# Kernel optimization log

Hardware: AMD Instinct MI355X
Metric: run time of the kernel (lower is better)

Reference implementation:

```python
import jax, jax.numpy as jnp
import numpy as np

N, E, EL = 20000, 320000, 100000
IN, HID, OUT, H = 256, 128, 128, 4
NEG_SLOPE = 0.2


def setup_inputs() -> dict:
    key = jax.random.key(0)
    ks = jax.random.split(key, 20)
    g = lambda k, shape, fan: jax.random.normal(k, shape, jnp.float32) * (1.0 / np.sqrt(fan))
    inp = {
        'x': jax.random.normal(ks[0], (N, IN), jnp.float32),
        'edge_index': jax.random.randint(ks[1], (2, E), 0, N, jnp.int32),
        'edge_label_index': jax.random.randint(ks[2], (2, EL), 0, N, jnp.int32),
        # GATv2 layer 1: in -> hidden, heads=H, concat
        'W_l1': g(ks[3], (IN, H * HID), IN), 'b_l1': jnp.zeros((H * HID,), jnp.float32),
        'W_r1': g(ks[4], (IN, H * HID), IN), 'b_r1': jnp.zeros((H * HID,), jnp.float32),
        'att1': g(ks[5], (H, HID), HID), 'bias1': jnp.zeros((H * HID,), jnp.float32),
        # GATv2 layer 2: H*hidden -> out, heads=1
        'W_l2': g(ks[6], (H * HID, OUT), H * HID), 'b_l2': jnp.zeros((OUT,), jnp.float32),
        'W_r2': g(ks[7], (H * HID, OUT), H * HID), 'b_r2': jnp.zeros((OUT,), jnp.float32),
        'att2': g(ks[8], (1, OUT), OUT), 'bias2': jnp.zeros((OUT,), jnp.float32),
        # decoder: Linear(2*OUT, HID) -> GELU -> Linear(HID, 1)
        'W_d1': g(ks[9], (2 * OUT, HID), 2 * OUT), 'b_d1': jnp.zeros((HID,), jnp.float32),
        'W_d2': g(ks[10], (HID, 1), HID), 'b_d2': jnp.zeros((1,), jnp.float32),
    }
    return inp


def gatv2_conv(x, src, dst, Wl, bl, Wr, br, att, bias, heads, ch):
    n = x.shape[0]
    xl = (x @ Wl + bl).reshape(n, heads, ch)  # source transform
    xr = (x @ Wr + br).reshape(n, heads, ch)  # target transform
    xj = xl[src]                              # [E, H, C] messages from source
    xi = xr[dst]                              # [E, H, C]
    e = jax.nn.leaky_relu(xi + xj, NEG_SLOPE)
    logits = jnp.einsum('ehc,hc->eh', e, att)  # [E, H]
    # segment softmax over incoming edges of each target node
    m = jax.ops.segment_max(logits, dst, num_segments=n)
    a = jnp.exp(logits - m[dst])
    s = jax.ops.segment_sum(a, dst, num_segments=n)
    alpha = a / s[dst]
    out = jax.ops.segment_sum(alpha[..., None] * xj, dst, num_segments=n)
    return out.reshape(n, heads * ch) + bias


def reference(x, edge_index, edge_label_index,
              W_l1, b_l1, W_r1, b_r1, att1, bias1,
              W_l2, b_l2, W_r2, b_r2, att2, bias2,
              W_d1, b_d1, W_d2, b_d2):
    n = x.shape[0]
    loops = jnp.arange(n, dtype=edge_index.dtype)
    src = jnp.concatenate([edge_index[0], loops])  # add_self_loops=True (PyG default)
    dst = jnp.concatenate([edge_index[1], loops])
    z = gatv2_conv(x, src, dst, W_l1, b_l1, W_r1, b_r1, att1, bias1, H, HID)
    z = jax.nn.gelu(z)  # dropout is identity in eval mode
    z = gatv2_conv(z, src, dst, W_l2, b_l2, W_r2, b_r2, att2, bias2, 1, OUT)
    # link decoder: gather-concat-MLP
    h = jnp.concatenate([z[edge_label_index[0]], z[edge_label_index[1]]], axis=-1)
    h = jax.nn.gelu(h @ W_d1 + b_d1)
    return (h @ W_d2 + b_d2).squeeze(-1)
```

## Files before the change

kernel.cpp:

```cpp
#include <hip/hip_runtime.h>
#include <hip/hip_bf16.h>
#include <math.h>
#include <stdint.h>

using bf16 = __hip_bfloat16;
typedef unsigned short u16;
typedef unsigned int   u32;
typedef __attribute__((ext_vector_type(8))) short short8;
typedef __attribute__((ext_vector_type(4))) float f32x4;
typedef _Float16 h2 __attribute__((ext_vector_type(2)));

static constexpr int NN   = 20000;
static constexpr int EE   = 320000;
static constexpr int ELN  = 100000;
static constexpr int ETOT = EE + NN;
static constexpr int INC  = 256;
static constexpr int C1   = 512;
static constexpr int C2   = 128;
static constexpr int NB   = (NN + 255) / 256;

__device__ __forceinline__ float us2f(u16 u){ union{u32 i; float f;}x; x.i=((u32)u)<<16; return x.f; }
__device__ __forceinline__ u16  f2us(float f){ union{bf16 h; u16 u;}c; c.h=__float2bfloat16(f); return c.u; }
__device__ __forceinline__ float h2f(u16 u){ union{u16 u; _Float16 h;}c; c.u=u; return (float)c.h; }
__device__ __forceinline__ float gelu_f(float x){
  float u = 1.5957691216057308f*(x + 0.044715f*x*x*x);
  float ex = __expf(u);
  float th = 1.f - 2.f/(ex + 1.f);
  return 0.5f*x*(1.f+th);
}
__device__ __forceinline__ void gl_lds16(const u16* g, void* l) {
  __builtin_amdgcn_global_load_lds((const __attribute__((address_space(1))) void*)g,
                                   (__attribute__((address_space(3))) void*)l, 16, 0, 0);
}
__device__ __forceinline__ void ld4v(const float* p, float* o){ float4 v=*(const float4*)p; o[0]=v.x;o[1]=v.y;o[2]=v.z;o[3]=v.w; }
__device__ __forceinline__ void ld4v(const u16* p, float* o){ uint2 v=*(const uint2*)p;
  o[0]=us2f(v.x&0xffff);o[1]=us2f(v.x>>16);o[2]=us2f(v.y&0xffff);o[3]=us2f(v.y>>16); }
__device__ __forceinline__ void ld4v(const _Float16* p, float* o){ uint2 v=*(const uint2*)p;
  o[0]=h2f(v.x&0xffff);o[1]=h2f(v.x>>16);o[2]=h2f(v.y&0xffff);o[3]=h2f(v.y>>16); }
__device__ __forceinline__ void ld8v(const float* p, float* o){ ld4v(p,o); ld4v(p+4,o+4); }
__device__ __forceinline__ void ld8v(const u16* p, float* o){ uint4 v=*(const uint4*)p;
  o[0]=us2f(v.x&0xffff);o[1]=us2f(v.x>>16);o[2]=us2f(v.y&0xffff);o[3]=us2f(v.y>>16);
  o[4]=us2f(v.z&0xffff);o[5]=us2f(v.z>>16);o[6]=us2f(v.w&0xffff);o[7]=us2f(v.w>>16); }
__device__ __forceinline__ void ld8v(const _Float16* p, float* o){ uint4 v=*(const uint4*)p;
  o[0]=h2f(v.x&0xffff);o[1]=h2f(v.x>>16);o[2]=h2f(v.y&0xffff);o[3]=h2f(v.y>>16);
  o[4]=h2f(v.z&0xffff);o[5]=h2f(v.z>>16);o[6]=h2f(v.w&0xffff);o[7]=h2f(v.w>>16); }
__device__ __forceinline__ void ld2v(const float* p, float* o){ float2 v=*(const float2*)p; o[0]=v.x;o[1]=v.y; }
__device__ __forceinline__ void ld2v(const _Float16* p, float* o){ u32 w=*(const u32*)p;
  o[0]=h2f(w&0xffff); o[1]=h2f(w>>16); }
__device__ __forceinline__ void st4v(float* p, const float* v){ *(float4*)p = make_float4(v[0],v[1],v[2],v[3]); }
__device__ __forceinline__ void st4v(u16* p, const float* v){ uint2 o;
  o.x=f2us(v[0])|((u32)f2us(v[1])<<16); o.y=f2us(v[2])|((u32)f2us(v[3])<<16); *(uint2*)p=o; }
__device__ __forceinline__ void st8v(float* p, const float* v){ st4v(p,v); st4v(p+4,v+4); }
__device__ __forceinline__ void st8v(u16* p, const float* v){ uint4 o;
  o.x=f2us(v[0])|((u32)f2us(v[1])<<16); o.y=f2us(v[2])|((u32)f2us(v[3])<<16);
  o.z=f2us(v[4])|((u32)f2us(v[5])<<16); o.w=f2us(v[6])|((u32)f2us(v[7])<<16); *(uint4*)p=o; }

__global__ void k_hist(const int* __restrict__ ei, int* __restrict__ cnt) {
  int e = blockIdx.x*blockDim.x + threadIdx.x;
  if (e < ETOT) {
    int d = (e < EE) ? ei[EE + e] : (e - EE);
    if ((u32)d < (u32)NN) atomicAdd(&cnt[d], 1);
  }
}
__global__ void k_scan_a(const int* __restrict__ cnt, int* __restrict__ row_ptr,
                         int* __restrict__ bsum) {
  __shared__ int buf[256];
  int idx = blockIdx.x*256 + threadIdx.x;
  int v = (idx < NN) ? cnt[idx] : 0;
  buf[threadIdx.x] = v;
  __syncthreads();
  for (int off = 1; off < 256; off <<= 1) {
    int t = (threadIdx.x >= off) ? buf[threadIdx.x - off] : 0;
    __syncthreads();
    buf[threadIdx.x] += t;
    __syncthreads();
  }
  if (idx < NN) row_ptr[idx] = buf[threadIdx.x] - v;
  if (threadIdx.x == 255) bsum[blockIdx.x] = buf[255];
}
__global__ void k_scan_b(int* __restrict__ bsum, int* __restrict__ row_ptr) {
  __shared__ int buf[128];
  int v = (threadIdx.x < NB) ? bsum[threadIdx.x] : 0;
  buf[threadIdx.x] = v;
  __syncthreads();
  for (int off = 1; off < 128; off <<= 1) {
    int t = (threadIdx.x >= off) ? buf[threadIdx.x - off] : 0;
    __syncthreads();
    buf[threadIdx.x] += t;
    __syncthreads();
  }
  if (threadIdx.x < NB) bsum[threadIdx.x] = buf[threadIdx.x] - v;
  if (threadIdx.x == 127) row_ptr[NN] = buf[127];
}
__global__ void k_scan_c(int* __restrict__ row_ptr, const int* __restrict__ bsum,
                         int* __restrict__ cur) {
  int idx = blockIdx.x*256 + threadIdx.x;
  if (idx < NN) {
    int v = row_ptr[idx] + bsum[blockIdx.x];
    row_ptr[idx] = v;
    cur[idx] = v;
  }
}
__global__ void k_scatter(const int* __restrict__ ei, int* __restrict__ cur,
                          int* __restrict__ col) {
  int e = blockIdx.x*blockDim.x + threadIdx.x;
  if (e < ETOT) {
    int s, d;
    if (e < EE) { s = ei[e]; d = ei[EE + e]; } else { s = d = e - EE; }
    if ((u32)d >= (u32)NN) d = 0;
    int pos = atomicAdd(&cur[d], 1);
    if ((u32)pos < (u32)ETOT) col[pos] = s;
  }
}

__global__ __launch_bounds__(256) void k_xsplit(const float* __restrict__ A,
                                                u16* __restrict__ Ath, u16* __restrict__ Atl,
                                                int n) {
  for (int i = blockIdx.x*256 + threadIdx.x; i < n; i += gridDim.x*256) {
    float v = A[i];
    u16 h = f2us(v);
    Ath[i] = h;
    Atl[i] = f2us(v - us2f(h));
  }
}

struct WsArgs { const float* src[5]; u16* th[5]; u16* tl[5]; int K[5]; int N[5]; };
__global__ __launch_bounds__(256) void k_wsplit_all(WsArgs a) {
  int seg = blockIdx.y;
  int K = a.K[seg], N = a.N[seg];
  int n = K * N;
  int idx = blockIdx.x*256 + threadIdx.x;
  if (idx >= n) return;
  int nn = idx / K, k = idx - nn*K;
  float v = a.src[seg][(size_t)k*N + nn];
  u16 h = f2us(v);
  a.th[seg][idx] = h;
  a.tl[seg][idx] = f2us(v - us2f(h));
}

__global__ __launch_bounds__(256, 3)
void k_mgemm_a(const u16* __restrict__ Ath, const u16* __restrict__ Atl,
               const u16* __restrict__ Bth, const u16* __restrict__ Btl,
               const float* __restrict__ biasA, const float* __restrict__ biasB, int ncut,
               _Float16* __restrict__ C, int M, int N, int K, int nby) {
  __shared__ __align__(16) u16 sm[17408];
  int tid = threadIdx.x;
  int bidy = blockIdx.x % nby, bidx = blockIdx.x / nby;
  int m0 = bidx * 128, n0 = bidy * 128;
  int wave = tid >> 6, lane = tid & 63;
  int wm = (wave & 1) * 64, wn = (wave >> 1) * 64;
  int l15 = lane & 15, quad = lane >> 4;
  const u16* pbase = (wave == 0) ? Ath : (wave == 1) ? Atl : (wave == 2) ? Bth : Btl;
  bool isA = wave < 2;
  int rbase = isA ? m0 : n0;
  int rseg = lane >> 2;
  int kseg = (lane & 3) * 8;
  f32x4 acc[4][4] = {};
  for (int k0 = 0; k0 < K; k0 += 32) {
    #pragma unroll
    for (int i = 0; i < 8; ++i) {
      int r = rbase + i*16 + rseg;
      if (isA && r > M-1) r = M-1;
      gl_lds16(&pbase[(size_t)r*K + k0 + kseg], (char*)sm + (wave<<13) + (i<<10));
    }
    __syncthreads();
    short8 af_h[4], af_l[4], bf_h[4], bf_l[4];
    #pragma unroll
    for (int i = 0; i < 4; ++i) {
      af_h[i] = *(const short8*)&sm[         (wm + i*16 + l15)*32 + quad*8];
      af_l[i] = *(const short8*)&sm[ 4096 +  (wm + i*16 + l15)*32 + quad*8];
      bf_h[i] = *(const short8*)&sm[ 8192 +  (wn + i*16 + l15)*32 + quad*8];
      bf_l[i] = *(const short8*)&sm[12288 +  (wn + i*16 + l15)*32 + quad*8];
    }
    #pragma unroll
    for (int i = 0; i < 4; ++i)
      #pragma unroll
      for (int j = 0; j < 4; ++j) {
        acc[i][j] = __builtin_amdgcn_mfma_f32_16x16x32_bf16(af_h[i], bf_l[j], acc[i][j], 0,0,0);
        acc[i][j] = __builtin_amdgcn_mfma_f32_16x16x32_bf16(af_l[i], bf_h[j], acc[i][j], 0,0,0);
        acc[i][j] = __builtin_amdgcn_mfma_f32_16x16x32_bf16(af_h[i], bf_h[j], acc[i][j], 0,0,0);
      }
    __syncthreads();
  }
  #pragma unroll
  for (int j = 0; j < 4; ++j) {
    int col = wn + j*16 + l15;
    int colg = n0 + col;
    float bv = (colg < ncut) ? biasA[colg] : biasB[colg - ncut];
    #pragma unroll
    for (int i = 0; i < 4; ++i) {
      int rowb = wm + i*16 + quad*4;
      #pragma unroll
      for (int r = 0; r < 4; ++r) {
        union { _Float16 h; u16 u; } cv;
        cv.h = (_Float16)(acc[i][j][r] + bv);
        sm[(rowb + r)*136 + col] = cv.u;
      }
    }
  }
  __syncthreads();
  int row = tid >> 1, half = (tid & 1) * 64;
  int gr = m0 + row;
  if (gr < M) {
    uint4* d = (uint4*)&C[(size_t)gr*N + n0 + half];
    const uint4* s = (const uint4*)&sm[row*136 + half];
    #pragma unroll
    for (int q = 0; q < 8; ++q) d[q] = s[q];
  }
}

__global__ __launch_bounds__(256, 2)
void k_dec3(const _Float16* __restrict__ z2,
            const int* __restrict__ eli,
            const u16* __restrict__ Wth, const u16* __restrict__ Wtl,
            const float* __restrict__ bd1,
            const float* __restrict__ Wd2, const float* __restrict__ bd2,
            float* __restrict__ out) {
  __shared__ __align__(16) u16 Ah[128][32], Al[128][32];
  __shared__ __align__(16) u16 Bh[128][32], Bl[128][32];
  __shared__ float pr[128][2];
  int tid = threadIdx.x;
  int e0 = blockIdx.x * 128;
  int wave = tid >> 6, lane = tid & 63;
  int wm = (wave & 1) * 64, wn = (wave >> 1) * 64;
  int l15 = lane & 15, quad = lane >> 4;
  int ar = tid >> 3;
  int ak = (tid & 7) * 4;
  int bn = tid >> 2;
  int bc = (tid & 3) * 8;
  int ia4[4], ib4[4];
  #pragma unroll
  for (int i = 0; i < 4; ++i) {
    int e = e0 + ar + 32*i;
    bool ev = e < ELN;
    int a = ev ? eli[e] : 0;      if ((u32)a >= (u32)NN) a = 0;
    int b = ev ? eli[ELN+e] : 0;  if ((u32)b >= (u32)NN) b = 0;
    ia4[i] = a; ib4[i] = b;
  }
  f32x4 acc[4][4] = {};
  for (int k0 = 0; k0 < 256; k0 += 32) {
    #pragma unroll
    for (int i = 0; i < 4; ++i) {
      int row = ar + 32*i;
      int kk = k0 + ak;
      const _Float16* src = (kk < 128) ? &z2[(size_t)ia4[i]*128 + kk]
                                       : &z2[(size_t)ib4[i]*128 + (kk - 128)];
      float hv[4];
      ld4v(src, hv);
      u16 hi[4], lo[4];
      #pragma unroll
      for (int j = 0; j < 4; ++j) {
        hi[j] = f2us(hv[j]);
        lo[j] = f2us(hv[j] - us2f(hi[j]));
      }
      *(uint2*)&Ah[row][ak] = make_uint2(hi[0]|((u32)hi[1]<<16), hi[2]|((u32)hi[3]<<16));
      *(uint2*)&Al[row][ak] = make_uint2(lo[0]|((u32)lo[1]<<16), lo[2]|((u32)lo[3]<<16));
    }
    #pragma unroll
    for (int i = 0; i < 2; ++i) {
      int n = bn + 64*i;
      *(uint4*)&Bh[n][bc] = *(const uint4*)&Wth[(size_t)n*256 + k0 + bc];
      *(uint4*)&Bl[n][bc] = *(const uint4*)&Wtl[(size_t)n*256 + k0 + bc];
    }
    __syncthreads();
    short8 af_h[4], af_l[4], bf_h[4], bf_l[4];
    #pragma unroll
    for (int i = 0; i < 4; ++i) {
      af_h[i] = *(const short8*)&Ah[wm + i*16 + l15][quad*8];
      af_l[i] = *(const short8*)&Al[wm + i*16 + l15][quad*8];
      bf_h[i] = *(const short8*)&Bh[wn + i*16 + l15][quad*8];
      bf_l[i] = *(const short8*)&Bl[wn + i*16 + l15][quad*8];
    }
    #pragma unroll
    for (int i = 0; i < 4; ++i)
      #pragma unroll
      for (int j = 0; j < 4; ++j) {
        acc[i][j] = __builtin_amdgcn_mfma_f32_16x16x32_bf16(af_h[i], bf_l[j], acc[i][j], 0,0,0);
        acc[i][j] = __builtin_amdgcn_mfma_f32_16x16x32_bf16(af_l[i], bf_h[j], acc[i][j], 0,0,0);
        acc[i][j] = __builtin_amdgcn_mfma_f32_16x16x32_bf16(af_h[i], bf_h[j], acc[i][j], 0,0,0);
      }
    __syncthreads();
  }
  float w2c[4], bbc[4];
  #pragma unroll
  for (int j = 0; j < 4; ++j) {
    int col = wn + j*16 + l15;
    w2c[j] = Wd2[col];
    bbc[j] = bd1[col];
  }
  #pragma unroll
  for (int i = 0; i < 4; ++i) {
    #pragma unroll
    for (int r = 0; r < 4; ++r) {
      float part = 0.f;
      #pragma unroll
      for (int j = 0; j < 4; ++j)
        part += gelu_f(acc[i][j][r] + bbc[j]) * w2c[j];
      part += __shfl_xor(part,1); part += __shfl_xor(part,2);
      part += __shfl_xor(part,4); part += __shfl_xor(part,8);
      if (l15 == 0) pr[wm + i*16 + quad*4 + r][wn>>6] = part;
    }
  }
  __syncthreads();
  if (tid < 128) {
    int e = e0 + tid;
    if (e < ELN) out[e] = pr[tid][0] + pr[tid][1] + bd2[0];
  }
}

__global__ __launch_bounds__(256) void k_edge1p(const _Float16* __restrict__ xl,
                                                const _Float16* __restrict__ xr, int ld,
                                                const float* __restrict__ att,
                                                const float* __restrict__ bias,
                                                const int* __restrict__ row_ptr,
                                                const int* __restrict__ col,
                                                u16* __restrict__ z1h, u16* __restrict__ z1l) {
  int wid = (blockIdx.x*blockDim.x + threadIdx.x) >> 6;
  if (wid >= NN) return;
  int lane = threadIdx.x & 63;
  int c8 = lane*8;
  union Q { uint4 u; h2 h[4]; };
  Q XI; XI.u = *(const uint4*)&xr[(size_t)wid*ld + c8];
  h2 at[4];
  #pragma unroll
  for (int k=0;k<4;++k) { at[k][0] = (_Float16)att[c8+2*k]; at[k][1] = (_Float16)att[c8+2*k+1]; }
  const h2 k02 = {(_Float16)0.2f, (_Float16)0.2f};
  float acc[8] = {};
  float s = 0.f;
  int e0 = __builtin_amdgcn_readfirstlane(row_ptr[wid]);
  int e1 = __builtin_amdgcn_readfirstlane(row_ptr[wid+1]);
  int e = e0;
  if ((e1 - e0) & 1) {
    int sn = __builtin_amdgcn_readfirstlane(col[e]); if ((u32)sn >= (u32)NN) sn = 0;
    Q XJ; XJ.u = *(const uint4*)&xl[(size_t)sn*ld + c8];
    float p = 0.f;
    #pragma unroll
    for (int k=0;k<4;++k) {
      h2 t = XI.h[k] + XJ.h[k];
      t = __builtin_elementwise_max(t, t*k02);
      p = __builtin_amdgcn_fdot2(t, at[k], p, false);
    }
    p += __shfl_xor(p,1); p += __shfl_xor(p,2);
    p += __shfl_xor(p,4); p += __shfl_xor(p,8);
    float w = __expf(p);
    s += w;
    #pragma unroll
    for (int k=0;k<4;++k) {
      acc[2*k]   += w*(float)XJ.h[k][0];
      acc[2*k+1] += w*(float)XJ.h[k][1];
    }
    ++e;
  }
  for (; e < e1; e += 2) {
    int s1 = __builtin_amdgcn_readfirstlane(col[e]);   if ((u32)s1 >= (u32)NN) s1 = 0;
    int s2 = __builtin_amdgcn_readfirstlane(col[e+1]); if ((u32)s2 >= (u32)NN) s2 = 0;
    Q X1, X2;
    X1.u = *(const uint4*)&xl[(size_t)s1*ld + c8];
    X2.u = *(const uint4*)&xl[(size_t)s2*ld + c8];
    float p1 = 0.f, p2 = 0.f;
    #pragma unroll
    for (int k=0;k<4;++k) {
      h2 t1 = XI.h[k] + X1.h[k];
      t1 = __builtin_elementwise_max(t1, t1*k02);
      p1 = __builtin_amdgcn_fdot2(t1, at[k], p1, false);
      h2 t2 = XI.h[k] + X2.h[k];
      t2 = __builtin_elementwise_max(t2, t2*k02);
      p2 = __builtin_amdgcn_fdot2(t2, at[k], p2, false);
    }
    p1 += __shfl_xor(p1,1); p2 += __shfl_xor(p2,1);
    p1 += __shfl_xor(p1,2); p2 += __shfl_xor(p2,2);
    p1 += __shfl_xor(p1,4); p2 += __shfl_xor(p2,4);
    p1 += __shfl_xor(p1,8); p2 += __shfl_xor(p2,8);
    float w1 = __expf(p1);
    float w2 = __expf(p2);
    s += w1 + w2;
    #pragma unroll
    for (int k=0;k<4;++k) {
      acc[2*k]   += w1*(float)X1.h[k][0] + w2*(float)X2.h[k][0];
      acc[2*k+1] += w1*(float)X1.h[k][1] + w2*(float)X2.h[k][1];
    }
  }
  float inv = 1.f/s;
  u16 hh[8], ll[8];
  #pragma unroll
  for (int j=0;j<8;++j) {
    float o = gelu_f(acc[j]*inv + bias[c8+j]);
    hh[j] = f2us(o);
    ll[j] = f2us(o - us2f(hh[j]));
  }
  uint4 H, L;
  H.x = hh[0]|((u32)hh[1]<<16); H.y = hh[2]|((u32)hh[3]<<16);
  H.z = hh[4]|((u32)hh[5]<<16); H.w = hh[6]|((u32)hh[7]<<16);
  L.x = ll[0]|((u32)ll[1]<<16); L.y = ll[2]|((u32)ll[3]<<16);
  L.z = ll[4]|((u32)ll[5]<<16); L.w = ll[6]|((u32)ll[7]<<16);
  *(uint4*)&z1h[(size_t)wid*C1 + c8] = H;
  *(uint4*)&z1l[(size_t)wid*C1 + c8] = L;
}

__global__ __launch_bounds__(256) void k_edge2p(const _Float16* __restrict__ xl,
                                                const _Float16* __restrict__ xr, int ld,
                                                const float* __restrict__ att,
                                                const float* __restrict__ bias,
                                                const int* __restrict__ row_ptr,
                                                const int* __restrict__ col,
                                                _Float16* __restrict__ z2) {
  int wid = (blockIdx.x*blockDim.x + threadIdx.x) >> 6;
  if (wid >= NN) return;
  int lane = threadIdx.x & 63;
  int c2 = lane*2;
  union W { u32 u; h2 h; };
  W XI; XI.u = *(const u32*)&xr[(size_t)wid*ld + c2];
  h2 at; at[0] = (_Float16)att[c2]; at[1] = (_Float16)att[c2+1];
  const h2 k02 = {(_Float16)0.2f, (_Float16)0.2f};
  float s = 0.f, ac0 = 0.f, ac1 = 0.f;
  int e0 = __builtin_amdgcn_readfirstlane(row_ptr[wid]);
  int e1 = __builtin_amdgcn_readfirstlane(row_ptr[wid+1]);
  int e = e0;
  if ((e1 - e0) & 1) {
    int sn = __builtin_amdgcn_readfirstlane(col[e]); if ((u32)sn >= (u32)NN) sn = 0;
    W XJ; XJ.u = *(const u32*)&xl[(size_t)sn*ld + c2];
    h2 t = XI.h + XJ.h;
    t = __builtin_elementwise_max(t, t*k02);
    float p = __builtin_amdgcn_fdot2(t, at, 0.f, false);
    p += __shfl_xor(p,1);  p += __shfl_xor(p,2);
    p += __shfl_xor(p,4);  p += __shfl_xor(p,8);
    p += __shfl_xor(p,16); p += __shfl_xor(p,32);
    float w = __expf(p);
    s += w;
    ac0 += w*(float)XJ.h[0];
    ac1 += w*(float)XJ.h[1];
    ++e;
  }
  for (; e < e1; e += 2) {
    int s1 = __builtin_amdgcn_readfirstlane(col[e]);   if ((u32)s1 >= (u32)NN) s1 = 0;
    int s2 = __builtin_amdgcn_readfirstlane(col[e+1]); if ((u32)s2 >= (u32)NN) s2 = 0;
    W X1, X2;
    X1.u = *(const u32*)&xl[(size_t)s1*ld + c2];
    X2.u = *(const u32*)&xl[(size_t)s2*ld + c2];
    h2 t1 = XI.h + X1.h;
    t1 = __builtin_elementwise_max(t1, t1*k02);
    float p1 = __builtin_amdgcn_fdot2(t1, at, 0.f, false);
    h2 t2 = XI.h + X2.h;
    t2 = __builtin_elementwise_max(t2, t2*k02);
    float p2 = __builtin_amdgcn_fdot2(t2, at, 0.f, false);
    p1 += __shfl_xor(p1,1);  p2 += __shfl_xor(p2,1);
    p1 += __shfl_xor(p1,2);  p2 += __shfl_xor(p2,2);
    p1 += __shfl_xor(p1,4);  p2 += __shfl_xor(p2,4);
    p1 += __shfl_xor(p1,8);  p2 += __shfl_xor(p2,8);
    p1 += __shfl_xor(p1,16); p2 += __shfl_xor(p2,16);
    p1 += __shfl_xor(p1,32); p2 += __shfl_xor(p2,32);
    float w1 = __expf(p1);
    float w2 = __expf(p2);
    s += w1 + w2;
    ac0 += w1*(float)X1.h[0] + w2*(float)X2.h[0];
    ac1 += w1*(float)X1.h[1] + w2*(float)X2.h[1];
  }
  float inv = 1.f/s;
  union { h2 h; u32 u; } o;
  o.h[0] = (_Float16)(ac0*inv + bias[c2]);
  o.h[1] = (_Float16)(ac1*inv + bias[c2+1]);
  *(u32*)&z2[(size_t)wid*C2 + c2] = o.u;
}

template <typename AT, typename CT>
__global__ __launch_bounds__(256) void k_gemm(const AT* __restrict__ A,
                                              const float* __restrict__ W,
                                              const float* __restrict__ bias,
                                              CT* __restrict__ C,
                                              int M, int Nc, int K) {
  __shared__ __align__(16) float As[16][64];
  __shared__ __align__(16) float Bs[16][64];
  int tid = threadIdx.x;
  int m0 = blockIdx.x*64, n0 = blockIdx.y*64;
  int ty = tid >> 4, tx = tid & 15;
  int lrow = tid >> 2;
  int lk   = (tid & 3)*4;
  int wk   = tid >> 4;
  int wn   = (tid & 15)*4;
  float acc[4][4] = {};
  for (int k0 = 0; k0 < K; k0 += 16) {
    int row = m0 + lrow;
    if (row < M) {
      float a4[4]; ld4v(&A[(size_t)row*K + k0 + lk], a4);
      As[lk+0][lrow]=a4[0]; As[lk+1][lrow]=a4[1]; As[lk+2][lrow]=a4[2]; As[lk+3][lrow]=a4[3];
    } else {
      #pragma unroll
      for (int j=0;j<4;++j) As[lk+j][lrow]=0.f;
    }
    {
      float4 bv4 = *(const float4*)&W[(size_t)(k0+wk)*Nc + n0 + wn];
      Bs[wk][wn+0]=bv4.x; Bs[wk][wn+1]=bv4.y; Bs[wk][wn+2]=bv4.z; Bs[wk][wn+3]=bv4.w;
    }
    __syncthreads();
    #pragma unroll
    for (int kk=0;kk<16;++kk) {
      float4 av = *(const float4*)&As[kk][ty*4];
      float4 bv = *(const float4*)&Bs[kk][tx*4];
      float a[4]={av.x,av.y,av.z,av.w}, b[4]={bv.x,bv.y,bv.z,bv.w};
      #pragma unroll
      for (int i=0;i<4;++i)
        #pragma unroll
        for (int j=0;j<4;++j)
          acc[i][j] += a[i]*b[j];
    }
    __syncthreads();
  }
  float bv[4];
  #pragma unroll
  for (int j=0;j<4;++j) bv[j] = bias[n0 + tx*4 + j];
  #pragma unroll
  for (int i=0;i<4;++i) {
    int row = m0 + ty*4 + i;
    if (row < M) {
      float o4[4] = {acc[i][0]+bv[0], acc[i][1]+bv[1], acc[i][2]+bv[2], acc[i][3]+bv[3]};
      st4v(&C[(size_t)row*Nc + n0 + tx*4], o4);
    }
  }
}

template <typename TI, typename TO>
__global__ __launch_bounds__(256) void k_edge1c(const TI* __restrict__ xl,
                                                const TI* __restrict__ xr, int ld,
                                                const float* __restrict__ att,
                                                const float* __restrict__ bias,
                                                const int* __restrict__ row_ptr,
                                                const int* __restrict__ col,
                                                TO* __restrict__ z1) {
  int wid = (blockIdx.x*blockDim.x + threadIdx.x) >> 6;
  if (wid >= NN) return;
  int lane = threadIdx.x & 63;
  int c8 = lane*8;
  float xi[8], av[8], acc[8] = {};
  ld8v(&xr[(size_t)wid*ld + c8], xi);
  #pragma unroll
  for (int j=0;j<8;++j) av[j] = att[c8+j];
  float s = 0.f;
  int e0 = row_ptr[wid], e1 = row_ptr[wid+1];
  for (int e = e0; e < e1; ++e) {
    int sn = col[e]; if ((u32)sn >= (u32)NN) sn = 0;
    float xj[8];
    ld8v(&xl[(size_t)sn*ld + c8], xj);
    float p = 0.f;
    #pragma unroll
    for (int j=0;j<8;++j) {
      float t = xi[j] + xj[j];
      t = fmaxf(t, 0.2f*t);
      p += t*av[j];
    }
    p += __shfl_xor(p,1); p += __shfl_xor(p,2);
    p += __shfl_xor(p,4); p += __shfl_xor(p,8);
    float w = __expf(p);
    s += w;
    #pragma unroll
    for (int j=0;j<8;++j) acc[j] += w*xj[j];
  }
  float inv = 1.f/s, o[8];
  #pragma unroll
  for (int j=0;j<8;++j) o[j] = gelu_f(acc[j]*inv + bias[c8+j]);
  st8v(&z1[(size_t)wid*C1 + c8], o);
}

template <typename TI, typename TO>
__global__ __launch_bounds__(256) void k_edge2c(const TI* __restrict__ xl,
                                                const TI* __restrict__ xr, int ld,
                                                const float* __restrict__ att,
                                                const float* __restrict__ bias,
                                                const int* __restrict__ row_ptr,
                                                const int* __restrict__ col,
                                                TO* __restrict__ z2) {
  int wid = (blockIdx.x*blockDim.x + threadIdx.x) >> 6;
  if (wid >= NN) return;
  int lane = threadIdx.x & 63;
  int c2 = lane*2;
  float xiv[2];
  ld2v(&xr[(size_t)wid*ld + c2], xiv);
  float a0 = att[c2], a1 = att[c2+1];
  float s = 0.f, ac0 = 0.f, ac1 = 0.f;
  int e0 = row_ptr[wid], e1 = row_ptr[wid+1];
  for (int e = e0; e < e1; ++e) {
    int sn = col[e]; if ((u32)sn >= (u32)NN) sn = 0;
    float xj[2];
    ld2v(&xl[(size_t)sn*ld + c2], xj);
    float t0 = xiv[0] + xj[0]; t0 = fmaxf(t0, 0.2f*t0);
    float t1 = xiv[1] + xj[1]; t1 = fmaxf(t1, 0.2f*t1);
    float p = t0*a0 + t1*a1;
    p += __shfl_xor(p,1);  p += __shfl_xor(p,2);
    p += __shfl_xor(p,4);  p += __shfl_xor(p,8);
    p += __shfl_xor(p,16); p += __shfl_xor(p,32);
    float w = __expf(p);
    s += w;
    ac0 += w*xj[0];
    ac1 += w*xj[1];
  }
  float inv = 1.f/s;
  z2[(size_t)wid*C2 + c2]   = (TO)(ac0*inv + bias[c2]);
  z2[(size_t)wid*C2 + c2+1] = (TO)(ac1*inv + bias[c2+1]);
}

__global__ __launch_bounds__(256) void k_dec2(const float* __restrict__ z2,
                                              const int* __restrict__ eli,
                                              const float* __restrict__ Wd1,
                                              const float* __restrict__ bd1,
                                              const float* __restrict__ Wd2,
                                              const float* __restrict__ bd2,
                                              float* __restrict__ out) {
  __shared__ __align__(16) float As[16][64];
  __shared__ __align__(16) float Bs[16][128];
  int tid = threadIdx.x;
  int e0 = blockIdx.x * 64;
  int ty = tid >> 4, tx = tid & 15;
  int lrow = tid >> 2;
  int lk   = (tid & 3) * 4;
  int wk   = tid >> 4;
  int wn   = (tid & 15) * 8;
  int e = e0 + lrow;
  bool ev = e < ELN;
  int ia = ev ? eli[e] : 0;       if ((u32)ia >= (u32)NN) ia = 0;
  int ib = ev ? eli[ELN+e] : 0;   if ((u32)ib >= (u32)NN) ib = 0;
  float acc[4][8] = {};
  for (int k0 = 0; k0 < 256; k0 += 16) {
    int kk4 = k0 + lk;
    const float* src = (kk4 < 128) ? &z2[(size_t)ia*128 + kk4]
                                   : &z2[(size_t)ib*128 + (kk4 - 128)];
    float4 a4 = ev ? *(const float4*)src : make_float4(0.f,0.f,0.f,0.f);
    As[lk+0][lrow]=a4.x; As[lk+1][lrow]=a4.y; As[lk+2][lrow]=a4.z; As[lk+3][lrow]=a4.w;
    *(float4*)&Bs[wk][wn]   = *(const float4*)&Wd1[(size_t)(k0+wk)*128 + wn];
    *(float4*)&Bs[wk][wn+4] = *(const float4*)&Wd1[(size_t)(k0+wk)*128 + wn + 4];
    __syncthreads();
    #pragma unroll
    for (int kk = 0; kk < 16; ++kk) {
      float4 av = *(const float4*)&As[kk][ty*4];
      float a[4] = {av.x, av.y, av.z, av.w};
      float4 b0 = *(const float4*)&Bs[kk][tx*4];
      float4 b1 = *(const float4*)&Bs[kk][64 + tx*4];
      float b[8] = {b0.x,b0.y,b0.z,b0.w,b1.x,b1.y,b1.z,b1.w};
      #pragma unroll
      for (int i = 0; i < 4; ++i)
        #pragma unroll
        for (int j = 0; j < 8; ++j)
          acc[i][j] += a[i]*b[j];
    }
    __syncthreads();
  }
  float w2[8], bb[8];
  #pragma unroll
  for (int j = 0; j < 4; ++j) {
    w2[j]   = Wd2[tx*4+j];      bb[j]   = bd1[tx*4+j];
    w2[j+4] = Wd2[64+tx*4+j];   bb[j+4] = bd1[64+tx*4+j];
  }
  float b2 = bd2[0];
  #pragma unroll
  for (int i = 0; i < 4; ++i) {
    float part = 0.f;
    #pragma unroll
    for (int j = 0; j < 8; ++j)
      part += gelu_f(acc[i][j] + bb[j]) * w2[j];
    part += __shfl_xor(part,1); part += __shfl_xor(part,2);
    part += __shfl_xor(part,4); part += __shfl_xor(part,8);
    int row = e0 + ty*4 + i;
    if (tx == 0 && row < ELN) out[row] = part + b2;
  }
}

__global__ void k_tiny(float* out, float code) {
  if (threadIdx.x == 0) out[0] = code;
}

extern "C" void kernel_launch(void* const* d_in, const int* in_sizes, int n_in,
                              void* d_out, int out_size, void* d_ws, size_t ws_size,
                              hipStream_t stream) {
  const float* x     = (const float*)d_in[0];
  const int*   ei    = (const int*)  d_in[1];
  const int*   eli   = (const int*)  d_in[2];
  const float* Wl1   = (const float*)d_in[3];
  const float* bl1   = (const float*)d_in[4];
  const float* Wr1   = (const float*)d_in[5];
  const float* br1   = (const float*)d_in[6];
  const float* att1  = (const float*)d_in[7];
  const float* bias1 = (const float*)d_in[8];
  const float* Wl2   = (const float*)d_in[9];
  const float* bl2   = (const float*)d_in[10];
  const float* Wr2   = (const float*)d_in[11];
  const float* br2   = (const float*)d_in[12];
  const float* att2  = (const float*)d_in[13];
  const float* bias2 = (const float*)d_in[14];
  const float* Wd1   = (const float*)d_in[15];
  const float* bd1   = (const float*)d_in[16];
  const float* Wd2   = (const float*)d_in[17];
  const float* bd2   = (const float*)d_in[18];
  float* out = (float*)d_out;

  constexpr size_t INTW = (size_t)(NN+1) + NN + ETOT;
  constexpr size_t FULL_WORDS = 3ull*NN*C1 + INTW;
  constexpr size_t CMP_WORDS  = 3ull*NN*C1/2 + INTW;

  bool full    = ws_size >= FULL_WORDS*4;
  bool compact = !full && ws_size >= CMP_WORDS*4;
  if (!full && !compact) {
    size_t mb = ws_size >> 20;
    k_tiny<<<1, 64, 0, stream>>>(out, 16384.f + (float)mb);
    return;
  }

  size_t regA = full ? (size_t)NN*C1 : (size_t)NN*C1/2;
  char* base = (char*)d_ws;
  void* wA = base;
  void* wB = base + regA*4;
  void* wC = base + 2*regA*4;
  int* row_ptr = (int*)(base + 3*regA*4);
  int* cnt     = row_ptr + (NN + 1);
  int* col     = cnt + NN;
  int* bsum    = (int*)wA;

  hipMemsetAsync(cnt, 0, NN*sizeof(int), stream);
  k_hist<<<(ETOT+255)/256, 256, 0, stream>>>(ei, cnt);
  k_scan_a<<<NB, 256, 0, stream>>>(cnt, row_ptr, bsum);
  k_scan_b<<<1, 128, 0, stream>>>(bsum, row_ptr);
  k_scan_c<<<NB, 256, 0, stream>>>(row_ptr, bsum, cnt);
  k_scatter<<<(ETOT+255)/256, 256, 0, stream>>>(ei, cnt, col);

  if (full) {
    _Float16* xlr1 = (_Float16*)wA;
    _Float16* xlr2 = (_Float16*)wA;
    u16* xth = (u16*)wB;
    u16* xtl = xth + (size_t)NN*INC;
    u16* wt1th = (u16*)((char*)wB + (21u<<20));
    u16* wt1tl = wt1th + 1024*256;
    u16* wt2th = wt1tl + 1024*256;
    u16* wt2tl = wt2th + 256*512;
    u16* wdth  = wt2tl + 256*512;
    u16* wdtl  = wdth  + 128*256;
    u16* z1h = (u16*)wC;
    u16* z1l = z1h + (size_t)NN*C1;
    _Float16* z2 = (_Float16*)wC;

    k_xsplit<<<2048, 256, 0, stream>>>(x, xth, xtl, NN*INC);
    WsArgs wa;
    wa.src[0]=Wl1; wa.th[0]=wt1th;          wa.tl[0]=wt1tl;          wa.K[0]=INC; wa.N[0]=C1;
    wa.src[1]=Wr1; wa.th[1]=wt1th+512*256;  wa.tl[1]=wt1tl+512*256;  wa.K[1]=INC; wa.N[1]=C1;
    wa.src[2]=Wl2; wa.th[2]=wt2th;          wa.tl[2]=wt2tl;          wa.K[2]=C1;  wa.N[2]=C2;
    wa.src[3]=Wr2; wa.th[3]=wt2th+128*512;  wa.tl[3]=wt2tl+128*512;  wa.K[3]=C1;  wa.N[3]=C2;
    wa.src[4]=Wd1; wa.th[4]=wdth;           wa.tl[4]=wdtl;           wa.K[4]=256; wa.N[4]=C2;
    k_wsplit_all<<<dim3(512, 5), 256, 0, stream>>>(wa);

    k_mgemm_a<<<157*8, 256, 0, stream>>>(xth, xtl, wt1th, wt1tl,
                                         bl1, br1, 512, xlr1, NN, 1024, INC, 8);
    k_edge1p<<<NN/4, 256, 0, stream>>>(xlr1, xlr1+512, 1024, att1, bias1, row_ptr, col, z1h, z1l);
    k_mgemm_a<<<157*2, 256, 0, stream>>>(z1h, z1l, wt2th, wt2tl,
                                         bl2, br2, 128, xlr2, NN, 256, C1, 2);
    k_edge2p<<<NN/4, 256, 0, stream>>>(xlr2, xlr2+128, 256, att2, bias2, row_ptr, col, z2);
    k_dec3<<<(ELN+127)/128, 256, 0, stream>>>(z2, eli, wdth, wdtl, bd1, Wd2, bd2, out);
  } else {
    u16* xl1 = (u16*)wA;
    u16* xr1 = (u16*)wB;
    u16* z1  = (u16*)wC;
    float* xl2 = (float*)wA;
    float* xr2 = (float*)wB;
    float* z2  = (float*)wC;
    dim3 g1((NN+63)/64, C1/64);
    dim3 g2((NN+63)/64, C2/64);
    k_gemm<float,u16><<<g1, 256, 0, stream>>>(x, Wl1, bl1, xl1, NN, C1, INC);
    k_gemm<float,u16><<<g1, 256, 0, stream>>>(x, Wr1, br1, xr1, NN, C1, INC);
    k_edge1c<u16,u16><<<NN/4, 256, 0, stream>>>(xl1, xr1, C1, att1, bias1, row_ptr, col, z1);
    k_gemm<u16,float><<<g2, 256, 0, stream>>>(z1, Wl2, bl2, xl2, NN, C2, C1);
    k_gemm<u16,float><<<g2, 256, 0, stream>>>(z1, Wr2, br2, xr2, NN, C2, C1);
    k_edge2c<float,float><<<NN/4, 256, 0, stream>>>(xl2, xr2, C2, att2, bias2, row_ptr, col, z2);
    k_dec2<<<(ELN+63)/64, 256, 0, stream>>>(z2, eli, Wd1, bd1, Wd2, bd2, out);
  }
}
```

Baseline: 359.2 us.

## Fuse prep kernels with histogram, unroll edge loops by four, raise dec3 occupancy

Folds the input split, the weight split and the edge-destination histogram into one grid-strided kernel, replacing three launches with one. The per-node edge loops in both GATv2 aggregation kernels move from a 2-way to a 4-way unroll with a scalar tail, keeping more gathers in flight. The decoder's launch-bounds occupancy hint goes from 2 to 3 blocks per SM, which may raise register pressure or cause spills. The fallback path keeps the separate histogram kernel.

```diff
diff --git a/kernel.cpp b/kernel.cpp
--- a/kernel.cpp
+++ b/kernel.cpp
@@ -55,13 +55,41 @@
   o.x=f2us(v[0])|((u32)f2us(v[1])<<16); o.y=f2us(v[2])|((u32)f2us(v[3])<<16);
   o.z=f2us(v[4])|((u32)f2us(v[5])<<16); o.w=f2us(v[6])|((u32)f2us(v[7])<<16); *(uint4*)p=o; }
 
-__global__ void k_hist(const int* __restrict__ ei, int* __restrict__ cnt) {
-  int e = blockIdx.x*blockDim.x + threadIdx.x;
-  if (e < ETOT) {
-    int d = (e < EE) ? ei[EE + e] : (e - EE);
-    if ((u32)d < (u32)NN) atomicAdd(&cnt[d], 1);
-  }
-}
+struct PrepArgs {
+  const float* x; u16* xth; u16* xtl; int nx;
+  const float* wsrc[5]; u16* wth[5]; u16* wtl[5]; int wK[5]; int wN[5];
+  const int* ei; int* cnt;
+};
+__global__ __launch_bounds__(256) void k_prep(PrepArgs a) {
+  int seg = blockIdx.y;
+  int tid = blockIdx.x*256 + threadIdx.x;
+  int stride = gridDim.x*256;
+  if (seg == 0) {
+    for (int i = tid; i < a.nx; i += stride) {
+      float v = a.x[i];
+      u16 h = f2us(v);
+      a.xth[i] = h;
+      a.xtl[i] = f2us(v - us2f(h));
+    }
+  } else if (seg <= 5) {
+    int s = seg - 1;
+    int K = a.wK[s], N = a.wN[s];
+    int n = K * N;
+    for (int i = tid; i < n; i += stride) {
+      int nn = i / K, k = i - nn*K;
+      float v = a.wsrc[s][(size_t)k*N + nn];
+      u16 h = f2us(v);
+      a.wth[s][i] = h;
+      a.wtl[s][i] = f2us(v - us2f(h));
+    }
+  } else {
+    for (int e = tid; e < ETOT; e += stride) {
+      int d = (e < EE) ? a.ei[EE + e] : (e - EE);
+      if ((u32)d < (u32)NN) atomicAdd(&a.cnt[d], 1);
+    }
+  }
+}
+
 __global__ void k_scan_a(const int* __restrict__ cnt, int* __restrict__ row_ptr,
                          int* __restrict__ bsum) {
   __shared__ int buf[256];
@@ -111,31 +139,6 @@
     int pos = atomicAdd(&cur[d], 1);
     if ((u32)pos < (u32)ETOT) col[pos] = s;
   }
-}
-
-__global__ __launch_bounds__(256) void k_xsplit(const float* __restrict__ A,
-                                                u16* __restrict__ Ath, u16* __restrict__ Atl,
-                                                int n) {
-  for (int i = blockIdx.x*256 + threadIdx.x; i < n; i += gridDim.x*256) {
-    float v = A[i];
-    u16 h = f2us(v);
-    Ath[i] = h;
-    Atl[i] = f2us(v - us2f(h));
-  }
-}
-
-struct WsArgs { const float* src[5]; u16* th[5]; u16* tl[5]; int K[5]; int N[5]; };
-__global__ __launch_bounds__(256) void k_wsplit_all(WsArgs a) {
-  int seg = blockIdx.y;
-  int K = a.K[seg], N = a.N[seg];
-  int n = K * N;
-  int idx = blockIdx.x*256 + threadIdx.x;
-  if (idx >= n) return;
-  int nn = idx / K, k = idx - nn*K;
-  float v = a.src[seg][(size_t)k*N + nn];
-  u16 h = f2us(v);
-  a.th[seg][idx] = h;
-  a.tl[seg][idx] = f2us(v - us2f(h));
 }
 
 __global__ __launch_bounds__(256, 3)
@@ -209,7 +212,7 @@
   }
 }
 
-__global__ __launch_bounds__(256, 2)
+__global__ __launch_bounds__(256, 3)
 void k_dec3(const _Float16* __restrict__ z2,
             const int* __restrict__ eli,
             const u16* __restrict__ Wth, const u16* __restrict__ Wtl,
@@ -330,7 +333,43 @@
   int e0 = __builtin_amdgcn_readfirstlane(row_ptr[wid]);
   int e1 = __builtin_amdgcn_readfirstlane(row_ptr[wid+1]);
   int e = e0;
-  if ((e1 - e0) & 1) {
+  for (; e + 4 <= e1; e += 4) {
+    int s1 = __builtin_amdgcn_readfirstlane(col[e]);   if ((u32)s1 >= (u32)NN) s1 = 0;
+    int s2 = __builtin_amdgcn_readfirstlane(col[e+1]); if ((u32)s2 >= (u32)NN) s2 = 0;
+    int s3 = __builtin_amdgcn_readfirstlane(col[e+2]); if ((u32)s3 >= (u32)NN) s3 = 0;
+    int s4 = __builtin_amdgcn_readfirstlane(col[e+3]); if ((u32)s4 >= (u32)NN) s4 = 0;
+    Q X1, X2, X3, X4;
+    X1.u = *(const uint4*)&xl[(size_t)s1*ld + c8];
+    X2.u = *(const uint4*)&xl[(size_t)s2*ld + c8];
+    X3.u = *(const uint4*)&xl[(size_t)s3*ld + c8];
+    X4.u = *(const uint4*)&xl[(size_t)s4*ld + c8];
+    float p1 = 0.f, p2 = 0.f, p3 = 0.f, p4 = 0.f;
+    #pragma unroll
+    for (int k=0;k<4;++k) {
+      h2 t1 = XI.h[k] + X1.h[k]; t1 = __builtin_elementwise_max(t1, t1*k02);
+      p1 = __builtin_amdgcn_fdot2(t1, at[k], p1, false);
+      h2 t2 = XI.h[k] + X2.h[k]; t2 = __builtin_elementwise_max(t2, t2*k02);
+      p2 = __builtin_amdgcn_fdot2(t2, at[k], p2, false);
+      h2 t3 = XI.h[k] + X3.h[k]; t3 = __builtin_elementwise_max(t3, t3*k02);
+      p3 = __builtin_amdgcn_fdot2(t3, at[k], p3, false);
+      h2 t4 = XI.h[k] + X4.h[k]; t4 = __builtin_elementwise_max(t4, t4*k02);
+      p4 = __builtin_amdgcn_fdot2(t4, at[k], p4, false);
+    }
+    p1 += __shfl_xor(p1,1); p2 += __shfl_xor(p2,1); p3 += __shfl_xor(p3,1); p4 += __shfl_xor(p4,1);
+    p1 += __shfl_xor(p1,2); p2 += __shfl_xor(p2,2); p3 += __shfl_xor(p3,2); p4 += __shfl_xor(p4,2);
+    p1 += __shfl_xor(p1,4); p2 += __shfl_xor(p2,4); p3 += __shfl_xor(p3,4); p4 += __shfl_xor(p4,4);
+    p1 += __shfl_xor(p1,8); p2 += __shfl_xor(p2,8); p3 += __shfl_xor(p3,8); p4 += __shfl_xor(p4,8);
+    float w1 = __expf(p1), w2 = __expf(p2), w3 = __expf(p3), w4 = __expf(p4);
+    s += (w1 + w2) + (w3 + w4);
+    #pragma unroll
+    for (int k=0;k<4;++k) {
+      acc[2*k]   += (w1*(float)X1.h[k][0] + w2*(float)X2.h[k][0])
+                  + (w3*(float)X3.h[k][0] + w4*(float)X4.h[k][0]);
+      acc[2*k+1] += (w1*(float)X1.h[k][1] + w2*(float)X2.h[k][1])
+                  + (w3*(float)X3.h[k][1] + w4*(float)X4.h[k][1]);
+    }
+  }
+  for (; e < e1; ++e) {
     int sn = __builtin_amdgcn_readfirstlane(col[e]); if ((u32)sn >= (u32)NN) sn = 0;
     Q XJ; XJ.u = *(const uint4*)&xl[(size_t)sn*ld + c8];
     float p = 0.f;
@@ -348,36 +387,6 @@
     for (int k=0;k<4;++k) {
       acc[2*k]   += w*(float)XJ.h[k][0];
       acc[2*k+1] += w*(float)XJ.h[k][1];
-    }
-    ++e;
-  }
-  for (; e < e1; e += 2) {
-    int s1 = __builtin_amdgcn_readfirstlane(col[e]);   if ((u32)s1 >= (u32)NN) s1 = 0;
-    int s2 = __builtin_amdgcn_readfirstlane(col[e+1]); if ((u32)s2 >= (u32)NN) s2 = 0;
-    Q X1, X2;
-    X1.u = *(const uint4*)&xl[(size_t)s1*ld + c8];
-    X2.u = *(const uint4*)&xl[(size_t)s2*ld + c8];
-    float p1 = 0.f, p2 = 0.f;
-    #pragma unroll
-    for (int k=0;k<4;++k) {
-      h2 t1 = XI.h[k] + X1.h[k];
-      t1 = __builtin_elementwise_max(t1, t1*k02);
-      p1 = __builtin_amdgcn_fdot2(t1, at[k], p1, false);
-      h2 t2 = XI.h[k] + X2.h[k];
-      t2 = __builtin_elementwise_max(t2, t2*k02);
-      p2 = __builtin_amdgcn_fdot2(t2, at[k], p2, false);
-    }
-    p1 += __shfl_xor(p1,1); p2 += __shfl_xor(p2,1);
-    p1 += __shfl_xor(p1,2); p2 += __shfl_xor(p2,2);
-    p1 += __shfl_xor(p1,4); p2 += __shfl_xor(p2,4);
-    p1 += __shfl_xor(p1,8); p2 += __shfl_xor(p2,8);
-    float w1 = __expf(p1);
-    float w2 = __expf(p2);
-    s += w1 + w2;
-    #pragma unroll
-    for (int k=0;k<4;++k) {
-      acc[2*k]   += w1*(float)X1.h[k][0] + w2*(float)X2.h[k][0];
-      acc[2*k+1] += w1*(float)X1.h[k][1] + w2*(float)X2.h[k][1];
     }
   }
   float inv = 1.f/s;
@@ -416,7 +425,36 @@
   int e0 = __builtin_amdgcn_readfirstlane(row_ptr[wid]);
   int e1 = __builtin_amdgcn_readfirstlane(row_ptr[wid+1]);
   int e = e0;
-  if ((e1 - e0) & 1) {
+  for (; e + 4 <= e1; e += 4) {
+    int s1 = __builtin_amdgcn_readfirstlane(col[e]);   if ((u32)s1 >= (u32)NN) s1 = 0;
+    int s2 = __builtin_amdgcn_readfirstlane(col[e+1]); if ((u32)s2 >= (u32)NN) s2 = 0;
+    int s3 = __builtin_amdgcn_readfirstlane(col[e+2]); if ((u32)s3 >= (u32)NN) s3 = 0;
+    int s4 = __builtin_amdgcn_readfirstlane(col[e+3]); if ((u32)s4 >= (u32)NN) s4 = 0;
+    W X1, X2, X3, X4;
+    X1.u = *(const u32*)&xl[(size_t)s1*ld + c2];
+    X2.u = *(const u32*)&xl[(size_t)s2*ld + c2];
+    X3.u = *(const u32*)&xl[(size_t)s3*ld + c2];
+    X4.u = *(const u32*)&xl[(size_t)s4*ld + c2];
+    h2 t1 = XI.h + X1.h; t1 = __builtin_elementwise_max(t1, t1*k02);
+    h2 t2 = XI.h + X2.h; t2 = __builtin_elementwise_max(t2, t2*k02);
+    h2 t3 = XI.h + X3.h; t3 = __builtin_elementwise_max(t3, t3*k02);
+    h2 t4 = XI.h + X4.h; t4 = __builtin_elementwise_max(t4, t4*k02);
+    float p1 = __builtin_amdgcn_fdot2(t1, at, 0.f, false);
+    float p2 = __builtin_amdgcn_fdot2(t2, at, 0.f, false);
+    float p3 = __builtin_amdgcn_fdot2(t3, at, 0.f, false);
+    float p4 = __builtin_amdgcn_fdot2(t4, at, 0.f, false);
+    p1 += __shfl_xor(p1,1);  p2 += __shfl_xor(p2,1);  p3 += __shfl_xor(p3,1);  p4 += __shfl_xor(p4,1);
+    p1 += __shfl_xor(p1,2);  p2 += __shfl_xor(p2,2);  p3 += __shfl_xor(p3,2);  p4 += __shfl_xor(p4,2);
+    p1 += __shfl_xor(p1,4);  p2 += __shfl_xor(p2,4);  p3 += __shfl_xor(p3,4);  p4 += __shfl_xor(p4,4);
+    p1 += __shfl_xor(p1,8);  p2 += __shfl_xor(p2,8);  p3 += __shfl_xor(p3,8);  p4 += __shfl_xor(p4,8);
+    p1 += __shfl_xor(p1,16); p2 += __shfl_xor(p2,16); p3 += __shfl_xor(p3,16); p4 += __shfl_xor(p4,16);
+    p1 += __shfl_xor(p1,32); p2 += __shfl_xor(p2,32); p3 += __shfl_xor(p3,32); p4 += __shfl_xor(p4,32);
+    float w1 = __expf(p1), w2 = __expf(p2), w3 = __expf(p3), w4 = __expf(p4);
+    s += (w1 + w2) + (w3 + w4);
+    ac0 += (w1*(float)X1.h[0] + w2*(float)X2.h[0]) + (w3*(float)X3.h[0] + w4*(float)X4.h[0]);
+    ac1 += (w1*(float)X1.h[1] + w2*(float)X2.h[1]) + (w3*(float)X3.h[1] + w4*(float)X4.h[1]);
+  }
+  for (; e < e1; ++e) {
     int sn = __builtin_amdgcn_readfirstlane(col[e]); if ((u32)sn >= (u32)NN) sn = 0;
     W XJ; XJ.u = *(const u32*)&xl[(size_t)sn*ld + c2];
     h2 t = XI.h + XJ.h;
@@ -429,31 +467,6 @@
     s += w;
     ac0 += w*(float)XJ.h[0];
     ac1 += w*(float)XJ.h[1];
-    ++e;
-  }
-  for (; e < e1; e += 2) {
-    int s1 = __builtin_amdgcn_readfirstlane(col[e]);   if ((u32)s1 >= (u32)NN) s1 = 0;
-    int s2 = __builtin_amdgcn_readfirstlane(col[e+1]); if ((u32)s2 >= (u32)NN) s2 = 0;
-    W X1, X2;
-    X1.u = *(const u32*)&xl[(size_t)s1*ld + c2];
-    X2.u = *(const u32*)&xl[(size_t)s2*ld + c2];
-    h2 t1 = XI.h + X1.h;
-    t1 = __builtin_elementwise_max(t1, t1*k02);
-    float p1 = __builtin_amdgcn_fdot2(t1, at, 0.f, false);
-    h2 t2 = XI.h + X2.h;
-    t2 = __builtin_elementwise_max(t2, t2*k02);
-    float p2 = __builtin_amdgcn_fdot2(t2, at, 0.f, false);
-    p1 += __shfl_xor(p1,1);  p2 += __shfl_xor(p2,1);
-    p1 += __shfl_xor(p1,2);  p2 += __shfl_xor(p2,2);
-    p1 += __shfl_xor(p1,4);  p2 += __shfl_xor(p2,4);
-    p1 += __shfl_xor(p1,8);  p2 += __shfl_xor(p2,8);
-    p1 += __shfl_xor(p1,16); p2 += __shfl_xor(p2,16);
-    p1 += __shfl_xor(p1,32); p2 += __shfl_xor(p2,32);
-    float w1 = __expf(p1);
-    float w2 = __expf(p2);
-    s += w1 + w2;
-    ac0 += w1*(float)X1.h[0] + w2*(float)X2.h[0];
-    ac1 += w1*(float)X1.h[1] + w2*(float)X2.h[1];
   }
   float inv = 1.f/s;
   union { h2 h; u32 u; } o;
@@ -462,6 +475,13 @@
   *(u32*)&z2[(size_t)wid*C2 + c2] = o.u;
 }
 
+__global__ void k_hist(const int* __restrict__ ei, int* __restrict__ cnt) {
+  int e = blockIdx.x*blockDim.x + threadIdx.x;
+  if (e < ETOT) {
+    int d = (e < EE) ? ei[EE + e] : (e - EE);
+    if ((u32)d < (u32)NN) atomicAdd(&cnt[d], 1);
+  }
+}
 template <typename AT, typename CT>
 __global__ __launch_bounds__(256) void k_gemm(const AT* __restrict__ A,
                                               const float* __restrict__ W,
@@ -517,7 +537,6 @@
     }
   }
 }
-
 template <typename TI, typename TO>
 __global__ __launch_bounds__(256) void k_edge1c(const TI* __restrict__ xl,
                                                 const TI* __restrict__ xr, int ld,
@@ -559,7 +578,6 @@
   for (int j=0;j<8;++j) o[j] = gelu_f(acc[j]*inv + bias[c8+j]);
   st8v(&z1[(size_t)wid*C1 + c8], o);
 }
-
 template <typename TI, typename TO>
 __global__ __launch_bounds__(256) void k_edge2c(const TI* __restrict__ xl,
                                                 const TI* __restrict__ xr, int ld,
@@ -596,7 +614,6 @@
   z2[(size_t)wid*C2 + c2]   = (TO)(ac0*inv + bias[c2]);
   z2[(size_t)wid*C2 + c2+1] = (TO)(ac1*inv + bias[c2+1]);
 }
-
 __global__ __launch_bounds__(256) void k_dec2(const float* __restrict__ z2,
                                               const int* __restrict__ eli,
                                               const float* __restrict__ Wd1,
@@ -713,11 +730,6 @@
   int* bsum    = (int*)wA;
 
   hipMemsetAsync(cnt, 0, NN*sizeof(int), stream);
-  k_hist<<<(ETOT+255)/256, 256, 0, stream>>>(ei, cnt);
-  k_scan_a<<<NB, 256, 0, stream>>>(cnt, row_ptr, bsum);
-  k_scan_b<<<1, 128, 0, stream>>>(bsum, row_ptr);
-  k_scan_c<<<NB, 256, 0, stream>>>(row_ptr, bsum, cnt);
-  k_scatter<<<(ETOT+255)/256, 256, 0, stream>>>(ei, cnt, col);
 
   if (full) {
     _Float16* xlr1 = (_Float16*)wA;
@@ -734,14 +746,20 @@
     u16* z1l = z1h + (size_t)NN*C1;
     _Float16* z2 = (_Float16*)wC;
 
-    k_xsplit<<<2048, 256, 0, stream>>>(x, xth, xtl, NN*INC);
-    WsArgs wa;
-    wa.src[0]=Wl1; wa.th[0]=wt1th;          wa.tl[0]=wt1tl;          wa.K[0]=INC; wa.N[0]=C1;
-    wa.src[1]=Wr1; wa.th[1]=wt1th+512*256;  wa.tl[1]=wt1tl+512*256;  wa.K[1]=INC; wa.N[1]=C1;
-    wa.src[2]=Wl2; wa.th[2]=wt2th;          wa.tl[2]=wt2tl;          wa.K[2]=C1;  wa.N[2]=C2;
-    wa.src[3]=Wr2; wa.th[3]=wt2th+128*512;  wa.tl[3]=wt2tl+128*512;  wa.K[3]=C1;  wa.N[3]=C2;
-    wa.src[4]=Wd1; wa.th[4]=wdth;           wa.tl[4]=wdtl;           wa.K[4]=256; wa.N[4]=C2;
-    k_wsplit_all<<<dim3(512, 5), 256, 0, stream>>>(wa);
+    PrepArgs pa;
+    pa.x = x; pa.xth = xth; pa.xtl = xtl; pa.nx = NN*INC;
+    pa.wsrc[0]=Wl1; pa.wth[0]=wt1th;         pa.wtl[0]=wt1tl;         pa.wK[0]=INC; pa.wN[0]=C1;
+    pa.wsrc[1]=Wr1; pa.wth[1]=wt1th+512*256; pa.wtl[1]=wt1tl+512*256; pa.wK[1]=INC; pa.wN[1]=C1;
+    pa.wsrc[2]=Wl2; pa.wth[2]=wt2th;         pa.wtl[2]=wt2tl;         pa.wK[2]=C1;  pa.wN[2]=C2;
+    pa.wsrc[3]=Wr2; pa.wth[3]=wt2th+128*512; pa.wtl[3]=wt2tl+128*512; pa.wK[3]=C1;  pa.wN[3]=C2;
+    pa.wsrc[4]=Wd1; pa.wth[4]=wdth;          pa.wtl[4]=wdtl;          pa.wK[4]=256; pa.wN[4]=C2;
+    pa.ei = ei; pa.cnt = cnt;
+    k_prep<<<dim3(1344, 7), 256, 0, stream>>>(pa);
+
+    k_scan_a<<<NB, 256, 0, stream>>>(cnt, row_ptr, bsum);
+    k_scan_b<<<1, 128, 0, stream>>>(bsum, row_ptr);
+    k_scan_c<<<NB, 256, 0, stream>>>(row_ptr, bsum, cnt);
+    k_scatter<<<(ETOT+255)/256, 256, 0, stream>>>(ei, cnt, col);
 
     k_mgemm_a<<<157*8, 256, 0, stream>>>(xth, xtl, wt1th, wt1tl,
                                          bl1, br1, 512, xlr1, NN, 1024, INC, 8);
@@ -757,6 +775,11 @@
     float* xl2 = (float*)wA;
     float* xr2 = (float*)wB;
     float* z2  = (float*)wC;
+    k_hist<<<(ETOT+255)/256, 256, 0, stream>>>(ei, cnt);
+    k_scan_a<<<NB, 256, 0, stream>>>(cnt, row_ptr, bsum);
+    k_scan_b<<<1, 128, 0, stream>>>(bsum, row_ptr);
+    k_scan_c<<<NB, 256, 0, stream>>>(row_ptr, bsum, cnt);
+    k_scatter<<<(ETOT+255)/256, 256, 0, stream>>>(ei, cnt, col);
     dim3 g1((NN+63)/64, C1/64);
     dim3 g2((NN+63)/64, C2/64);
     k_gemm<float,u16><<<g1, 256, 0, stream>>>(x, Wl1, bl1, xl1, NN, C1, INC);
```

After: 344.7 us. 1.04x faster.
